# Optimization experiments

Hardware: AMD Instinct MI355X
Metric: run time of the kernel (lower is better)

## Reference

```python
import jax, jax.numpy as jnp
import numpy as np

N = 50000      # nodes
E = 800000     # edges
G = 32         # graphs in batch
K = 16         # max current nodes per graph
F_IN = 128
HID = 64
HEADS = 4
NEG = -1e9
TEMPERATURE = 1.0


def setup_inputs() -> dict:
    key = jax.random.key(0)
    ks = jax.random.split(key, 16)
    inp = {
        "x": jax.random.normal(ks[0], (N, F_IN), dtype=jnp.float32),
        "edge_index": jax.random.randint(ks[1], (2, E), 0, N, dtype=jnp.int64) if jax.config.jax_enable_x64 else jax.random.randint(ks[1], (2, E), 0, N).astype(jnp.int32),
        "cur_nodes": jax.random.randint(ks[2], (G, K), 0, N).astype(jnp.int32),
        "cur_counts": jax.random.randint(ks[3], (G,), 0, K).astype(jnp.int32),
        "masks": jax.random.bernoulli(ks[4], 0.3, (G, N)),
        "W1": jax.random.normal(ks[5], (F_IN, HEADS * HID), dtype=jnp.float32) * 0.05,
        "att_src1": jax.random.normal(ks[6], (HEADS, HID), dtype=jnp.float32) * 0.05,
        "att_dst1": jax.random.normal(ks[7], (HEADS, HID), dtype=jnp.float32) * 0.05,
        "b1": jax.random.normal(ks[8], (HEADS * HID,), dtype=jnp.float32) * 0.05,
        "W2": jax.random.normal(ks[9], (HEADS * HID, HID), dtype=jnp.float32) * 0.05,
        "att_src2": jax.random.normal(ks[10], (1, HID), dtype=jnp.float32) * 0.05,
        "att_dst2": jax.random.normal(ks[11], (1, HID), dtype=jnp.float32) * 0.05,
        "b2": jax.random.normal(ks[12], (HID,), dtype=jnp.float32) * 0.05,
        "action_w": jax.random.normal(ks[13], (HID, 1), dtype=jnp.float32) * 0.01,
        "action_b": jnp.zeros((1,), dtype=jnp.float32),
        "stop_w": jax.random.normal(ks[14], (HID, 1), dtype=jnp.float32) * 0.01,
        "stop_b": jnp.zeros((1,), dtype=jnp.float32),
    }
    return inp


def gat_conv(x, src, dst, W, att_s, att_d, b, num_nodes):
    """PyG-style GATConv (add_self_loops already applied to src/dst)."""
    H, C = att_s.shape
    h = (x @ W).reshape(num_nodes, H, C)            # [N,H,C]
    a_s = jnp.sum(h * att_s[None], axis=-1)         # [N,H]
    a_d = jnp.sum(h * att_d[None], axis=-1)         # [N,H]
    e = jax.nn.leaky_relu(a_s[src] + a_d[dst], 0.2) # [E',H]
    m = jax.ops.segment_max(e, dst, num_segments=num_nodes)
    ex = jnp.exp(e - m[dst])
    denom = jax.ops.segment_sum(ex, dst, num_segments=num_nodes)
    coef = ex / denom[dst]                          # scatter-softmax over dst
    out = jax.ops.segment_sum(coef[:, :, None] * h[src], dst, num_segments=num_nodes)
    return out.reshape(num_nodes, H * C) + b


def reference(x, edge_index, cur_nodes, cur_counts, masks,
              W1, att_src1, att_dst1, b1, W2, att_src2, att_dst2, b2,
              action_w, action_b, stop_w, stop_b):
    num_nodes = x.shape[0]
    loops = jnp.arange(num_nodes, dtype=edge_index.dtype)
    src = jnp.concatenate([edge_index[0], loops])
    dst = jnp.concatenate([edge_index[1], loops])

    h = jax.nn.relu(gat_conv(x, src, dst, W1, att_src1, att_dst1, b1, num_nodes))
    h = gat_conv(h, src, dst, W2, att_src2, att_dst2, b2, num_nodes)  # [N,HID]

    node_scores = jnp.tanh(h @ action_w + action_b)[:, 0]             # [N]

    # per-graph masked gather-mean pooling over current nodes
    valid = (jnp.arange(K)[None, :] < cur_counts[:, None])            # [G,K]
    gathered = h[cur_nodes] * valid[:, :, None].astype(h.dtype)       # [G,K,HID]
    cnt = jnp.maximum(cur_counts, 1).astype(h.dtype)
    contexts = gathered.sum(axis=1) / cnt[:, None]                    # [G,HID]
    stop_scores = jnp.tanh(contexts @ stop_w + stop_b)                # [G,1]

    masked = jnp.where(masks, node_scores[None, :], NEG)              # [G,N]
    all_scores = jnp.concatenate([masked, stop_scores], axis=1) / TEMPERATURE
    probs = jax.nn.softmax(all_scores, axis=-1)                       # [G,N+1]

    stop = (cur_counts == 0)
    onehot = jnp.zeros((num_nodes + 1,), dtype=probs.dtype).at[num_nodes].set(1.0)
    return jnp.where(stop[:, None], onehot[None, :], probs)
```

## Files before the change

kernel.cpp:

```cpp
#include <hip/hip_runtime.h>
#include <hip/hip_runtime_api.h>

#define NNODES 50000
#define NEDGES 800000
#define GG 32
#define KCUR 16
#define FIN 128
#define HIDN 64
#define NHEADS 4
#define F1 256
#define NCHUNK 196
#define NBUCK 196
#define EPB 2048

typedef unsigned short u16;
typedef unsigned char u8;
typedef short bf8 __attribute__((ext_vector_type(8)));
typedef float f32x4 __attribute__((ext_vector_type(4)));
typedef float f32x2 __attribute__((ext_vector_type(2)));

__device__ __forceinline__ u16 f2bf(float f) {
    unsigned u = __float_as_uint(f);
    return (u16)((u + 0x7fffu + ((u >> 16) & 1u)) >> 16);
}
__device__ __forceinline__ float lrelu(float x) { return x > 0.f ? x : 0.2f * x; }
__device__ __forceinline__ unsigned pk4fp8(float a, float b, float c, float d) {
    unsigned u = __builtin_amdgcn_cvt_pk_fp8_f32(a, b, 0u, false);
    u = __builtin_amdgcn_cvt_pk_fp8_f32(c, d, u, true);
    return u;
}

__device__ __forceinline__ void fma16(uint4 hv, float ex, float* acc) {
    f32x2 c;
    c = __builtin_amdgcn_cvt_pk_f32_fp8(hv.x, false);
    acc[0]  = fmaf(ex, c.x, acc[0]);  acc[1]  = fmaf(ex, c.y, acc[1]);
    c = __builtin_amdgcn_cvt_pk_f32_fp8(hv.x, true);
    acc[2]  = fmaf(ex, c.x, acc[2]);  acc[3]  = fmaf(ex, c.y, acc[3]);
    c = __builtin_amdgcn_cvt_pk_f32_fp8(hv.y, false);
    acc[4]  = fmaf(ex, c.x, acc[4]);  acc[5]  = fmaf(ex, c.y, acc[5]);
    c = __builtin_amdgcn_cvt_pk_f32_fp8(hv.y, true);
    acc[6]  = fmaf(ex, c.x, acc[6]);  acc[7]  = fmaf(ex, c.y, acc[7]);
    c = __builtin_amdgcn_cvt_pk_f32_fp8(hv.z, false);
    acc[8]  = fmaf(ex, c.x, acc[8]);  acc[9]  = fmaf(ex, c.y, acc[9]);
    c = __builtin_amdgcn_cvt_pk_f32_fp8(hv.z, true);
    acc[10] = fmaf(ex, c.x, acc[10]); acc[11] = fmaf(ex, c.y, acc[11]);
    c = __builtin_amdgcn_cvt_pk_f32_fp8(hv.w, false);
    acc[12] = fmaf(ex, c.x, acc[12]); acc[13] = fmaf(ex, c.y, acc[13]);
    c = __builtin_amdgcn_cvt_pk_f32_fp8(hv.w, true);
    acc[14] = fmaf(ex, c.x, acc[14]); acc[15] = fmaf(ex, c.y, acc[15]);
}

__device__ __forceinline__ void fma8(uint2 hv, float ex, float* acc) {
    f32x2 c;
    c = __builtin_amdgcn_cvt_pk_f32_fp8(hv.x, false);
    acc[0] = fmaf(ex, c.x, acc[0]); acc[1] = fmaf(ex, c.y, acc[1]);
    c = __builtin_amdgcn_cvt_pk_f32_fp8(hv.x, true);
    acc[2] = fmaf(ex, c.x, acc[2]); acc[3] = fmaf(ex, c.y, acc[3]);
    c = __builtin_amdgcn_cvt_pk_f32_fp8(hv.y, false);
    acc[4] = fmaf(ex, c.x, acc[4]); acc[5] = fmaf(ex, c.y, acc[5]);
    c = __builtin_amdgcn_cvt_pk_f32_fp8(hv.y, true);
    acc[6] = fmaf(ex, c.x, acc[6]); acc[7] = fmaf(ex, c.y, acc[7]);
}

__global__ __launch_bounds__(256)
void pack_k(const float* __restrict__ W1, const float* __restrict__ W2,
            u16* __restrict__ W1p, u16* __restrict__ W2p)
{
    int idx = blockIdx.x * 256 + threadIdx.x;
    const float* src; u16* dst; int S, N, li;
    if (idx < 32768) { src = W1; dst = W1p; S = FIN / 32; N = F1; li = idx; }
    else if (idx < 49152) { src = W2; dst = W2p; S = F1 / 32; N = HIDN; li = idx - 32768; }
    else return;
    int j = li & 7, l = (li >> 3) & 63, rest = li >> 9;
    int s = rest % S, t = rest / S;
    int k = s * 32 + (l >> 4) * 8 + j;
    int n = t * 16 + (l & 15);
    dst[li] = f2bf(src[(size_t)k * N + n]);
}

__global__ __launch_bounds__(256)
void hist_k(const int* __restrict__ dst, int* __restrict__ deg)
{
    int e = blockIdx.x * 256 + threadIdx.x;
    if (e >= NEDGES) return;
    atomicAdd(&deg[dst[e]], 1);
}

__global__ __launch_bounds__(256)
void chunksum_k(const int* __restrict__ deg, int* __restrict__ csum)
{
    __shared__ int ws[4];
    int i = blockIdx.x * 256 + threadIdx.x;
    int v = (i < NNODES) ? deg[i] : 0;
#pragma unroll
    for (int o = 32; o; o >>= 1) v += __shfl_down(v, o);
    if ((threadIdx.x & 63) == 0) ws[threadIdx.x >> 6] = v;
    __syncthreads();
    if (threadIdx.x == 0) csum[blockIdx.x] = ws[0] + ws[1] + ws[2] + ws[3];
}

__global__ __launch_bounds__(256)
void expand_k(const int* __restrict__ deg, const int* __restrict__ csum,
              int* __restrict__ rowptr, int* __restrict__ bcur)
{
    __shared__ int ws[4], ws2[4];
    __shared__ int boff;
    int tid = threadIdx.x, lane = tid & 63, wid = tid >> 6;
    int v0 = (tid < blockIdx.x) ? csum[tid] : 0;
#pragma unroll
    for (int o = 32; o; o >>= 1) v0 += __shfl_down(v0, o);
    if (lane == 0) ws[wid] = v0;
    __syncthreads();
    if (tid == 0) boff = ws[0] + ws[1] + ws[2] + ws[3];
    __syncthreads();
    int i = blockIdx.x * 256 + tid;
    int v = (i < NNODES) ? deg[i] : 0;
    int x = v;
#pragma unroll
    for (int o = 1; o < 64; o <<= 1) {
        int y = __shfl_up(x, o);
        if (lane >= o) x += y;
    }
    if (lane == 63) ws2[wid] = x;
    __syncthreads();
    int off = boff;
    for (int w = 0; w < wid; w++) off += ws2[w];
    int excl = off + x - v;
    if (i < NNODES) {
        rowptr[i] = excl;
        if ((i & 255) == 0) bcur[i >> 8] = excl;
    }
    if (i == 0) rowptr[NNODES] = NEDGES;
}

__global__ __launch_bounds__(256)
void bin_k(const int* __restrict__ src, const int* __restrict__ dst,
           int* __restrict__ bcur, uint2* __restrict__ tmp)
{
    __shared__ int lcnt[NBUCK];
    __shared__ int lbase[NBUCK];
    int tid = threadIdx.x;
    int e0 = blockIdx.x * EPB;
    for (int i = tid; i < NBUCK; i += 256) lcnt[i] = 0;
    __syncthreads();
    int s_[8], d_[8], r_[8];
#pragma unroll
    for (int j = 0; j < 8; j++) {
        int e = e0 + j * 256 + tid;
        if (e < NEDGES) {
            s_[j] = src[e];
            d_[j] = dst[e];
            r_[j] = atomicAdd(&lcnt[d_[j] >> 8], 1);
        }
    }
    __syncthreads();
    for (int i = tid; i < NBUCK; i += 256)
        if (lcnt[i]) lbase[i] = atomicAdd(&bcur[i], lcnt[i]);
    __syncthreads();
#pragma unroll
    for (int j = 0; j < 8; j++) {
        int e = e0 + j * 256 + tid;
        if (e < NEDGES) {
            int b = d_[j] >> 8;
            tmp[lbase[b] + r_[j]] = make_uint2((unsigned)s_[j], (unsigned)d_[j]);
        }
    }
}

__global__ __launch_bounds__(1024)
void reorder_k(const int* __restrict__ rowptr, const uint2* __restrict__ tmp,
               int* __restrict__ csr)
{
    __shared__ int cur[256];
    int tid = threadIdx.x;
    int b = blockIdx.x;
    int n0 = b << 8;
    if (tid < 256) {
        int n = n0 + tid;
        cur[tid] = (n < NNODES) ? rowptr[n] : 0;
    }
    int base = rowptr[n0];
    int end = (b == NBUCK - 1) ? NEDGES : rowptr[n0 + 256];
    __syncthreads();
    for (int e = base + tid; e < end; e += 1024) {
        uint2 pr = tmp[e];
        int pos = atomicAdd(&cur[pr.y & 255], 1);
        csr[pos] = (int)pr.x;
    }
}

__global__ __launch_bounds__(256)
void gemm1_k(const float* __restrict__ X, const u16* __restrict__ Bp,
             const float* __restrict__ att_s, const float* __restrict__ att_d,
             u8* __restrict__ h1f8, float* __restrict__ as1, float* __restrict__ ad1)
{
    const int S = FIN / 32;
    int lane = threadIdx.x & 63, w = threadIdx.x >> 6;
    int m0 = blockIdx.x * 64;
    int row_in = lane & 15, kq = lane >> 4;
    f32x4 acc[4][4];
#pragma unroll
    for (int r = 0; r < 4; r++)
#pragma unroll
        for (int tt = 0; tt < 4; tt++) acc[r][tt] = (f32x4){0.f, 0.f, 0.f, 0.f};
    int R = (NNODES - m0) >> 4; if (R > 4) R = 4;

    for (int s = 0; s < S; s++) {
        bf8 bfrag[4];
#pragma unroll
        for (int tt = 0; tt < 4; tt++) {
            int t = w * 4 + tt;
            bfrag[tt] = *(const bf8*)(Bp + (((size_t)t * S + s) * 64 + lane) * 8);
        }
        int kb = s * 32 + kq * 8;
        bf8 af[4];
#pragma unroll
        for (int r = 0; r < 4; r++)
            if (r < R) {
                const float* xp = X + (size_t)(m0 + r * 16 + row_in) * FIN + kb;
                float4 x0 = *(const float4*)xp;
                float4 x1 = *(const float4*)(xp + 4);
                bf8 a;
                a[0] = (short)f2bf(x0.x); a[1] = (short)f2bf(x0.y);
                a[2] = (short)f2bf(x0.z); a[3] = (short)f2bf(x0.w);
                a[4] = (short)f2bf(x1.x); a[5] = (short)f2bf(x1.y);
                a[6] = (short)f2bf(x1.z); a[7] = (short)f2bf(x1.w);
                af[r] = a;
            }
#pragma unroll
        for (int r = 0; r < 4; r++)
            if (r < R)
#pragma unroll
                for (int tt = 0; tt < 4; tt++)
                    acc[r][tt] = __builtin_amdgcn_mfma_f32_16x16x32_bf16(bfrag[tt], af[r], acc[r][tt], 0, 0, 0);
    }
    float attS[16], attD[16];
#pragma unroll
    for (int tt = 0; tt < 4; tt++)
#pragma unroll
        for (int v = 0; v < 4; v++) {
            attS[tt * 4 + v] = att_s[w * 64 + tt * 16 + kq * 4 + v];
            attD[tt * 4 + v] = att_d[w * 64 + tt * 16 + kq * 4 + v];
        }
#pragma unroll
    for (int r = 0; r < 4; r++) {
        if (r >= R) break;
        int node = m0 + r * 16 + row_in;
        float pa = 0.f, pd = 0.f;
#pragma unroll
        for (int tt = 0; tt < 4; tt++) {
            unsigned u = pk4fp8(acc[r][tt][0], acc[r][tt][1], acc[r][tt][2], acc[r][tt][3]);
            *(unsigned*)(h1f8 + (size_t)node * F1 + (w * 4 + tt) * 16 + kq * 4) = u;
#pragma unroll
            for (int v = 0; v < 4; v++) {
                pa = fmaf(acc[r][tt][v], attS[tt * 4 + v], pa);
                pd = fmaf(acc[r][tt][v], attD[tt * 4 + v], pd);
            }
        }
        pa += __shfl_xor(pa, 16); pa += __shfl_xor(pa, 32);
        pd += __shfl_xor(pd, 16); pd += __shfl_xor(pd, 32);
        if (kq == 0) { as1[node * 4 + w] = pa; ad1[node * 4 + w] = pd; }
    }
}

__global__ __launch_bounds__(256)
void gagg1_gemm2(const int* __restrict__ rowptr, const int* __restrict__ csr,
                 const float* __restrict__ as1, const float* __restrict__ ad1,
                 const u8* __restrict__ h1f8, const float* __restrict__ b1,
                 const u16* __restrict__ W2p,
                 const float* __restrict__ att_s, const float* __restrict__ att_d,
                 u8* __restrict__ h2f8, float* __restrict__ as2, float* __restrict__ ad2)
{
    __shared__ unsigned rows[16 * 128];
    __shared__ float asl[4][16], adl[4][16];
    int tid = threadIdx.x;
    int wid = tid >> 6, lane = tid & 63;
    int q = lane >> 4, li = lane & 15;
    int dl = wid * 4 + q;
    int d0 = blockIdx.x * 16;
    int d = d0 + dl;
    int beg = rowptr[d];
    int tot = rowptr[d + 1] - beg + 1;
    int h = li >> 2;
    int c0 = li << 4;
    const int* rowm = csr + beg - 1;
    float adh = ad1[d * 4 + h];
    float den = 0.f;
    float acc[16];
#pragma unroll
    for (int j = 0; j < 16; j++) acc[j] = 0.f;

    int s0 = d;
    int s1 = (1 < tot) ? rowm[1] : d;
    int s2 = (2 < tot) ? rowm[2] : d;
    int s3 = (3 < tot) ? rowm[3] : d;
    int p = 0;
    while (p < tot) {
        float av0 = as1[((unsigned)s0 << 2) + h];
        float av1 = as1[((unsigned)s1 << 2) + h];
        float av2 = as1[((unsigned)s2 << 2) + h];
        float av3 = as1[((unsigned)s3 << 2) + h];
        uint4 h0 = *(const uint4*)(h1f8 + ((unsigned)s0 << 8) + c0);
        uint4 h1 = *(const uint4*)(h1f8 + ((unsigned)s1 << 8) + c0);
        uint4 h2 = *(const uint4*)(h1f8 + ((unsigned)s2 << 8) + c0);
        uint4 h3 = *(const uint4*)(h1f8 + ((unsigned)s3 << 8) + c0);
        int np = p + 4;
        int n0 = (np     < tot) ? rowm[np]     : d;
        int n1 = (np + 1 < tot) ? rowm[np + 1] : d;
        int n2 = (np + 2 < tot) ? rowm[np + 2] : d;
        int n3 = (np + 3 < tot) ? rowm[np + 3] : d;
        float e0 = __expf(lrelu(av0 + adh));
        float e1 = (p + 1 < tot) ? __expf(lrelu(av1 + adh)) : 0.f;
        float e2 = (p + 2 < tot) ? __expf(lrelu(av2 + adh)) : 0.f;
        float e3 = (p + 3 < tot) ? __expf(lrelu(av3 + adh)) : 0.f;
        den += e0 + e1 + e2 + e3;
        fma16(h0, e0, acc);
        fma16(h1, e1, acc);
        fma16(h2, e2, acc);
        fma16(h3, e3, acc);
        s0 = n0; s1 = n1; s2 = n2; s3 = n3;
        p = np;
    }

    {
        float rden = 1.f / den;
        float4 b0 = *(const float4*)(b1 + c0);
        float4 b4 = *(const float4*)(b1 + c0 + 4);
        float4 b8 = *(const float4*)(b1 + c0 + 8);
        float4 bc = *(const float4*)(b1 + c0 + 12);
        float bb[16] = {b0.x, b0.y, b0.z, b0.w, b4.x, b4.y, b4.z, b4.w,
                        b8.x, b8.y, b8.z, b8.w, bc.x, bc.y, bc.z, bc.w};
        unsigned r[8];
#pragma unroll
        for (int jj = 0; jj < 8; jj++) {
            float lo = fmaxf(fmaf(acc[2 * jj],     rden, bb[2 * jj]),     0.f);
            float hi = fmaxf(fmaf(acc[2 * jj + 1], rden, bb[2 * jj + 1]), 0.f);
            asm("v_cvt_pk_bf16_f32 %0, %1, %2" : "=v"(r[jj]) : "v"(lo), "v"(hi));
        }
        unsigned* rb = rows + dl * 128;
        int g0 = (2 * li) ^ (dl & 7);
        int g1 = (2 * li + 1) ^ (dl & 7);
        *(uint4*)(rb + g0 * 4) = make_uint4(r[0], r[1], r[2], r[3]);
        *(uint4*)(rb + g1 * 4) = make_uint4(r[4], r[5], r[6], r[7]);
    }
    __syncthreads();

    int row_in = li, kq = q;
    f32x4 acc2 = (f32x4){0.f, 0.f, 0.f, 0.f};
#pragma unroll
    for (int s = 0; s < 8; s++) {
        bf8 bfrag = *(const bf8*)(W2p + (((size_t)wid * 8 + s) * 64 + lane) * 8);
        int g = (4 * s + kq) ^ (row_in & 7);
        bf8 af = *(const bf8*)(rows + row_in * 128 + g * 4);
        acc2 = __builtin_amdgcn_mfma_f32_16x16x32_bf16(bfrag, af, acc2, 0, 0, 0);
    }
    int node = d0 + row_in;
    unsigned u = pk4fp8(acc2[0], acc2[1], acc2[2], acc2[3]);
    *(unsigned*)(h2f8 + (size_t)node * HIDN + wid * 16 + kq * 4) = u;
    float pa = 0.f, pd = 0.f;
#pragma unroll
    for (int v = 0; v < 4; v++) {
        pa = fmaf(acc2[v], att_s[wid * 16 + kq * 4 + v], pa);
        pd = fmaf(acc2[v], att_d[wid * 16 + kq * 4 + v], pd);
    }
    pa += __shfl_xor(pa, 16); pa += __shfl_xor(pa, 32);
    pd += __shfl_xor(pd, 16); pd += __shfl_xor(pd, 32);
    if (kq == 0) { asl[wid][row_in] = pa; adl[wid][row_in] = pd; }
    __syncthreads();
    if (tid < 16) {
        as2[d0 + tid] = asl[0][tid] + asl[1][tid] + asl[2][tid] + asl[3][tid];
        ad2[d0 + tid] = adl[0][tid] + adl[1][tid] + adl[2][tid] + adl[3][tid];
    }
}

__global__ __launch_bounds__(256)
void gagg2(const int* __restrict__ rowptr, const int* __restrict__ csr,
           const float* __restrict__ as2, const float* __restrict__ ad2,
           const u8* __restrict__ h2f8, const float* __restrict__ b2,
           const float* __restrict__ aw, const float* __restrict__ ab,
           float* __restrict__ outp, float* __restrict__ scores)
{
    int wid = threadIdx.x >> 6, lane = threadIdx.x & 63;
    int d = blockIdx.x * 4 + wid;
    if (d >= NNODES) return;
    int beg = rowptr[d];
    int tot = rowptr[d + 1] - beg + 1;
    int g8 = lane >> 3;
    int li = lane & 7;
    int c0 = li << 3;
    const int* rowm = csr + beg - 1;
    float adh = ad2[d];
    float den = 0.f;
    float acc[8];
#pragma unroll
    for (int j = 0; j < 8; j++) acc[j] = 0.f;

    int p = g8;
    while (p + 8 < tot) {
        int sa = (p == 0) ? d : rowm[p];
        int sb = rowm[p + 8];
        float ava = as2[sa], avb = as2[sb];
        uint2 ha = *(const uint2*)(h2f8 + ((unsigned)sa << 6) + c0);
        uint2 hb = *(const uint2*)(h2f8 + ((unsigned)sb << 6) + c0);
        float exa = __expf(lrelu(ava + adh));
        den += exa;
        fma8(ha, exa, acc);
        float exb = __expf(lrelu(avb + adh));
        den += exb;
        fma8(hb, exb, acc);
        p += 16;
    }
    if (p < tot) {
        int s = (p == 0) ? d : rowm[p];
        float av = as2[s];
        uint2 hv = *(const uint2*)(h2f8 + ((unsigned)s << 6) + c0);
        float ex = __expf(lrelu(av + adh));
        den += ex;
        fma8(hv, ex, acc);
    }

    den += __shfl_xor(den, 8); den += __shfl_xor(den, 16); den += __shfl_xor(den, 32);
#pragma unroll
    for (int j = 0; j < 8; j++) {
        acc[j] += __shfl_xor(acc[j], 8);
        acc[j] += __shfl_xor(acc[j], 16);
        acc[j] += __shfl_xor(acc[j], 32);
    }

    float rden = 1.f / den;
    float4 blo = *(const float4*)(b2 + c0);
    float4 bhi = *(const float4*)(b2 + c0 + 4);
    float o0 = fmaf(acc[0], rden, blo.x);
    float o1 = fmaf(acc[1], rden, blo.y);
    float o2 = fmaf(acc[2], rden, blo.z);
    float o3 = fmaf(acc[3], rden, blo.w);
    float o4 = fmaf(acc[4], rden, bhi.x);
    float o5 = fmaf(acc[5], rden, bhi.y);
    float o6 = fmaf(acc[6], rden, bhi.z);
    float o7 = fmaf(acc[7], rden, bhi.w);
    if (lane < 8) {
        *(float4*)(outp + (size_t)d * HIDN + c0) = make_float4(o0, o1, o2, o3);
        *(float4*)(outp + (size_t)d * HIDN + c0 + 4) = make_float4(o4, o5, o6, o7);
    }
    float4 alo = *(const float4*)(aw + c0);
    float4 ahi = *(const float4*)(aw + c0 + 4);
    float p_ = o0 * alo.x + o1 * alo.y + o2 * alo.z + o3 * alo.w
             + o4 * ahi.x + o5 * ahi.y + o6 * ahi.z + o7 * ahi.w;
    p_ += __shfl_xor(p_, 1); p_ += __shfl_xor(p_, 2); p_ += __shfl_xor(p_, 4);
    if (lane == 0) scores[d] = tanhf(p_ + ab[0]);
}

__global__ __launch_bounds__(256)
void partials_k(const float* __restrict__ scores, const int* __restrict__ masks,
                float* __restrict__ pmax, float* __restrict__ psum)
{
    __shared__ float lm[4], ls[4];
    int g = blockIdx.y;
    float m = -3.0e38f, s = 0.f;
    for (int n = blockIdx.x * 256 + threadIdx.x; n < NNODES; n += gridDim.x * 256) {
        if (masks[(size_t)g * NNODES + n]) {
            float v = scores[n];
            if (v > m) { s = s * __expf(m - v) + 1.f; m = v; }
            else s += __expf(v - m);
        }
    }
#pragma unroll
    for (int o = 1; o < 64; o <<= 1) {
        float om = __shfl_xor(m, o), os = __shfl_xor(s, o);
        float M = fmaxf(m, om);
        s = s * __expf(m - M) + os * __expf(om - M);
        m = M;
    }
    if ((threadIdx.x & 63) == 0) { lm[threadIdx.x >> 6] = m; ls[threadIdx.x >> 6] = s; }
    __syncthreads();
    if (threadIdx.x == 0) {
        float M = m, S = s;
        for (int w_ = 1; w_ < 4; w_++) {
            float M2 = fmaxf(M, lm[w_]);
            S = S * __expf(M - M2) + ls[w_] * __expf(lm[w_] - M2);
            M = M2;
        }
        pmax[g * 64 + blockIdx.x] = M;
        psum[g * 64 + blockIdx.x] = S;
    }
}

__global__ __launch_bounds__(64)
void combine_k(const float* __restrict__ hf, const int* __restrict__ cur_nodes,
               const int* __restrict__ cur_counts, const float* __restrict__ sw,
               const float* __restrict__ sb,
               const float* __restrict__ pmax, const float* __restrict__ psum,
               float* __restrict__ gmax, float* __restrict__ gsum,
               float* __restrict__ stops)
{
    int g = blockIdx.x, tid = threadIdx.x;
    int cnt = cur_counts[g];
    float s = 0.f;
    for (int k = 0; k < KCUR; k++)
        if (k < cnt) s += hf[(size_t)cur_nodes[g * KCUR + k] * HIDN + tid];
    float ctx = s / (float)(cnt > 1 ? cnt : 1);
    float p = ctx * sw[tid];
#pragma unroll
    for (int o = 1; o < 64; o <<= 1) p += __shfl_xor(p, o);
    float stop = tanhf(p + sb[0]);

    float m = pmax[g * 64 + tid], sm = psum[g * 64 + tid];
#pragma unroll
    for (int o = 1; o < 64; o <<= 1) {
        float om = __shfl_xor(m, o), os = __shfl_xor(sm, o);
        float M = fmaxf(m, om);
        sm = sm * __expf(m - M) + os * __expf(om - M);
        m = M;
    }
    if (tid == 0) {
        float M2 = fmaxf(m, stop);
        float S2 = sm * __expf(m - M2) + __expf(stop - M2);
        gmax[g] = M2; gsum[g] = S2; stops[g] = stop;
    }
}

__global__ __launch_bounds__(256)
void write_k(const float* __restrict__ scores, const int* __restrict__ masks,
             const float* __restrict__ gmax, const float* __restrict__ gsum,
             const float* __restrict__ stops, const int* __restrict__ cur_counts,
             float* __restrict__ out)
{
    int g = blockIdx.y;
    int j = blockIdx.x * 256 + threadIdx.x;
    if (j > NNODES) return;
    float v;
    if (cur_counts[g] == 0) {
        v = (j == NNODES) ? 1.f : 0.f;
    } else {
        float m = gmax[g];
        float Z = gsum[g];
        if (j == NNODES) v = __expf(stops[g] - m) / Z;
        else v = masks[(size_t)g * NNODES + j] ? __expf(scores[j] - m) / Z : 0.f;
    }
    out[(size_t)g * (NNODES + 1) + j] = v;
}

extern "C" void kernel_launch(void* const* d_in, const int* in_sizes, int n_in,
                              void* d_out, int out_size, void* d_ws, size_t ws_size,
                              hipStream_t stream) {
    const float* x        = (const float*)d_in[0];
    const int* ei         = (const int*)d_in[1];
    const int* cur_nodes  = (const int*)d_in[2];
    const int* cur_counts = (const int*)d_in[3];
    const int* masks      = (const int*)d_in[4];
    const float* W1       = (const float*)d_in[5];
    const float* att_s1   = (const float*)d_in[6];
    const float* att_d1   = (const float*)d_in[7];
    const float* b1       = (const float*)d_in[8];
    const float* W2       = (const float*)d_in[9];
    const float* att_s2   = (const float*)d_in[10];
    const float* att_d2   = (const float*)d_in[11];
    const float* b2       = (const float*)d_in[12];
    const float* action_w = (const float*)d_in[13];
    const float* action_b = (const float*)d_in[14];
    const float* stop_w   = (const float*)d_in[15];
    const float* stop_b   = (const float*)d_in[16];
    float* out = (float*)d_out;

    const int* srcp = ei;
    const int* dstp = ei + NEDGES;

    int* deg = (int*)d_ws;
    char* zend = (char*)(deg + NNODES);
    size_t zbytes = zend - (char*)d_ws;
    int* csum   = (int*)zend;
    int* rowptr = csum + 256;
    int* bcur   = rowptr + NNODES + 4;
    int* csr    = bcur + 256;
    u16* W1p    = (u16*)(csr + NEDGES);
    u16* W2p    = W1p + 32768;
    u8*  h1f8   = (u8*)(W2p + 16384);
    u8*  h2f8   = h1f8 + (size_t)NNODES * F1;
    float* as1  = (float*)(h2f8 + (size_t)NNODES * HIDN);
    float* ad1  = as1 + (size_t)NNODES * 4;
    float* as2  = ad1 + (size_t)NNODES * 4;
    float* ad2  = as2 + NNODES;
    float* hf   = ad2 + NNODES;
    float* scores = hf + (size_t)NNODES * HIDN;
    float* stops  = scores + NNODES;
    float* pmax = stops + GG;
    float* psum = pmax + GG * 64;
    float* gmax = psum + GG * 64;
    float* gsum = gmax + GG;
    size_t total = (char*)(gsum + GG) - (char*)d_ws;
    if (total > ws_size) return;

    uint2* tmp = (uint2*)hf;

    auto cdiv = [](long long a, long long b) { return (int)((a + b - 1) / b); };

    (void)hipMemsetAsync(deg, 0, zbytes, stream);

    hist_k<<<cdiv(NEDGES, 256), 256, 0, stream>>>(dstp, deg);
    chunksum_k<<<NCHUNK, 256, 0, stream>>>(deg, csum);
    expand_k<<<NCHUNK, 256, 0, stream>>>(deg, csum, rowptr, bcur);
    bin_k<<<cdiv(NEDGES, EPB), 256, 0, stream>>>(srcp, dstp, bcur, tmp);
    reorder_k<<<NBUCK, 1024, 0, stream>>>(rowptr, tmp, csr);

    pack_k<<<192, 256, 0, stream>>>(W1, W2, W1p, W2p);

    gemm1_k<<<cdiv(NNODES, 64), 256, 0, stream>>>(x, W1p, att_s1, att_d1, h1f8, as1, ad1);

    gagg1_gemm2<<<NNODES / 16, 256, 0, stream>>>(rowptr, csr, as1, ad1, h1f8, b1,
                                                 W2p, att_s2, att_d2, h2f8, as2, ad2);

    gagg2<<<cdiv(NNODES, 4), 256, 0, stream>>>(rowptr, csr, as2, ad2, h2f8, b2,
                                               action_w, action_b, hf, scores);

    partials_k<<<dim3(64, GG), 256, 0, stream>>>(scores, masks, pmax, psum);
    combine_k<<<GG, 64, 0, stream>>>(hf, cur_nodes, cur_counts, stop_w, stop_b,
                                     pmax, psum, gmax, gsum, stops);
    write_k<<<dim3(cdiv(NNODES + 1, 256), GG), 256, 0, stream>>>(scores, masks, gmax, gsum,
                                                                 stops, cur_counts, out);
}
```

Measured before the change: 282.4 us.

## Sort destination nodes by degree to balance aggregation work per block

Builds a degree histogram and counting-sort order of nodes, then has both aggregation kernels process nodes in that order, so that the nodes grouped into each block and wavefront have similar edge counts. This is meant to reduce load imbalance and divergence in the per-node edge loops. It adds two small kernels, an extra indirection on node index, and scattered writes of outputs instead of contiguous ones. The atomic-based ordering within a bin is nondeterministic but still covers every node exactly once.

```diff
diff --git a/kernel.cpp b/kernel.cpp
--- a/kernel.cpp
+++ b/kernel.cpp
@@ -12,6 +12,7 @@
 #define NCHUNK 196
 #define NBUCK 196
 #define EPB 2048
+#define DBIN 64
 
 typedef unsigned short u16;
 typedef unsigned char u8;
@@ -87,16 +88,52 @@
 }
 
 __global__ __launch_bounds__(256)
-void chunksum_k(const int* __restrict__ deg, int* __restrict__ csum)
+void chunksum_k(const int* __restrict__ deg, int* __restrict__ csum,
+                int* __restrict__ dhist)
 {
     __shared__ int ws[4];
+    __shared__ int lh[DBIN];
+    int tid = threadIdx.x;
+    if (tid < DBIN) lh[tid] = 0;
+    __syncthreads();
+    int i = blockIdx.x * 256 + tid;
+    int v = 0;
+    if (i < NNODES) {
+        v = deg[i];
+        atomicAdd(&lh[v < DBIN - 1 ? v : DBIN - 1], 1);
+    }
+#pragma unroll
+    for (int o = 32; o; o >>= 1) v += __shfl_down(v, o);
+    if ((tid & 63) == 0) ws[tid >> 6] = v;
+    __syncthreads();
+    if (tid == 0) csum[blockIdx.x] = ws[0] + ws[1] + ws[2] + ws[3];
+    if (tid < DBIN && lh[tid]) atomicAdd(&dhist[tid], lh[tid]);
+}
+
+__global__ __launch_bounds__(64)
+void dprefix_k(const int* __restrict__ dhist, int* __restrict__ dcur)
+{
+    int tid = threadIdx.x;
+    int v = dhist[tid];
+    int x = v;
+#pragma unroll
+    for (int o = 1; o < 64; o <<= 1) {
+        int y = __shfl_up(x, o);
+        if (tid >= o) x += y;
+    }
+    dcur[tid] = x - v;
+}
+
+__global__ __launch_bounds__(256)
+void dorder_k(const int* __restrict__ deg, int* __restrict__ dcur,
+              int* __restrict__ order)
+{
     int i = blockIdx.x * 256 + threadIdx.x;
-    int v = (i < NNODES) ? deg[i] : 0;
-#pragma unroll
-    for (int o = 32; o; o >>= 1) v += __shfl_down(v, o);
-    if ((threadIdx.x & 63) == 0) ws[threadIdx.x >> 6] = v;
-    __syncthreads();
-    if (threadIdx.x == 0) csum[blockIdx.x] = ws[0] + ws[1] + ws[2] + ws[3];
+    if (i >= NNODES) return;
+    int v = deg[i];
+    int b = v < DBIN - 1 ? v : DBIN - 1;
+    int pos = atomicAdd(&dcur[b], 1);
+    order[pos] = i;
 }
 
 __global__ __launch_bounds__(256)
@@ -264,7 +301,8 @@
 }
 
 __global__ __launch_bounds__(256)
-void gagg1_gemm2(const int* __restrict__ rowptr, const int* __restrict__ csr,
+void gagg1_gemm2(const int* __restrict__ order,
+                 const int* __restrict__ rowptr, const int* __restrict__ csr,
                  const float* __restrict__ as1, const float* __restrict__ ad1,
                  const u8* __restrict__ h1f8, const float* __restrict__ b1,
                  const u16* __restrict__ W2p,
@@ -278,7 +316,7 @@
     int q = lane >> 4, li = lane & 15;
     int dl = wid * 4 + q;
     int d0 = blockIdx.x * 16;
-    int d = d0 + dl;
+    int d = order[d0 + dl];
     int beg = rowptr[d];
     int tot = rowptr[d + 1] - beg + 1;
     int h = li >> 2;
@@ -346,6 +384,7 @@
     __syncthreads();
 
     int row_in = li, kq = q;
+    int nodeB = order[d0 + row_in];
     f32x4 acc2 = (f32x4){0.f, 0.f, 0.f, 0.f};
 #pragma unroll
     for (int s = 0; s < 8; s++) {
@@ -354,9 +393,8 @@
         bf8 af = *(const bf8*)(rows + row_in * 128 + g * 4);
         acc2 = __builtin_amdgcn_mfma_f32_16x16x32_bf16(bfrag, af, acc2, 0, 0, 0);
     }
-    int node = d0 + row_in;
     unsigned u = pk4fp8(acc2[0], acc2[1], acc2[2], acc2[3]);
-    *(unsigned*)(h2f8 + (size_t)node * HIDN + wid * 16 + kq * 4) = u;
+    *(unsigned*)(h2f8 + (size_t)nodeB * HIDN + wid * 16 + kq * 4) = u;
     float pa = 0.f, pd = 0.f;
 #pragma unroll
     for (int v = 0; v < 4; v++) {
@@ -368,21 +406,22 @@
     if (kq == 0) { asl[wid][row_in] = pa; adl[wid][row_in] = pd; }
     __syncthreads();
     if (tid < 16) {
-        as2[d0 + tid] = asl[0][tid] + asl[1][tid] + asl[2][tid] + asl[3][tid];
-        ad2[d0 + tid] = adl[0][tid] + adl[1][tid] + adl[2][tid] + adl[3][tid];
-    }
-}
-
-__global__ __launch_bounds__(256)
-void gagg2(const int* __restrict__ rowptr, const int* __restrict__ csr,
+        int nd = order[d0 + tid];
+        as2[nd] = asl[0][tid] + asl[1][tid] + asl[2][tid] + asl[3][tid];
+        ad2[nd] = adl[0][tid] + adl[1][tid] + adl[2][tid] + adl[3][tid];
+    }
+}
+
+__global__ __launch_bounds__(256)
+void gagg2(const int* __restrict__ order,
+           const int* __restrict__ rowptr, const int* __restrict__ csr,
            const float* __restrict__ as2, const float* __restrict__ ad2,
            const u8* __restrict__ h2f8, const float* __restrict__ b2,
            const float* __restrict__ aw, const float* __restrict__ ab,
            float* __restrict__ outp, float* __restrict__ scores)
 {
     int wid = threadIdx.x >> 6, lane = threadIdx.x & 63;
-    int d = blockIdx.x * 4 + wid;
-    if (d >= NNODES) return;
+    int d = order[blockIdx.x * 4 + wid];
     int beg = rowptr[d];
     int tot = rowptr[d + 1] - beg + 1;
     int g8 = lane >> 3;
@@ -566,12 +605,15 @@
     const int* dstp = ei + NEDGES;
 
     int* deg = (int*)d_ws;
-    char* zend = (char*)(deg + NNODES);
+    int* dhist = deg + NNODES;
+    char* zend = (char*)(dhist + DBIN);
     size_t zbytes = zend - (char*)d_ws;
     int* csum   = (int*)zend;
     int* rowptr = csum + 256;
     int* bcur   = rowptr + NNODES + 4;
-    int* csr    = bcur + 256;
+    int* dcur   = bcur + 256;
+    int* order  = dcur + DBIN;
+    int* csr    = order + NNODES;
     u16* W1p    = (u16*)(csr + NEDGES);
     u16* W2p    = W1p + 32768;
     u8*  h1f8   = (u8*)(W2p + 16384);
@@ -597,19 +639,21 @@
     (void)hipMemsetAsync(deg, 0, zbytes, stream);
 
     hist_k<<<cdiv(NEDGES, 256), 256, 0, stream>>>(dstp, deg);
-    chunksum_k<<<NCHUNK, 256, 0, stream>>>(deg, csum);
+    chunksum_k<<<NCHUNK, 256, 0, stream>>>(deg, csum, dhist);
     expand_k<<<NCHUNK, 256, 0, stream>>>(deg, csum, rowptr, bcur);
     bin_k<<<cdiv(NEDGES, EPB), 256, 0, stream>>>(srcp, dstp, bcur, tmp);
     reorder_k<<<NBUCK, 1024, 0, stream>>>(rowptr, tmp, csr);
+    dprefix_k<<<1, 64, 0, stream>>>(dhist, dcur);
+    dorder_k<<<NCHUNK, 256, 0, stream>>>(deg, dcur, order);
 
     pack_k<<<192, 256, 0, stream>>>(W1, W2, W1p, W2p);
 
     gemm1_k<<<cdiv(NNODES, 64), 256, 0, stream>>>(x, W1p, att_s1, att_d1, h1f8, as1, ad1);
 
-    gagg1_gemm2<<<NNODES / 16, 256, 0, stream>>>(rowptr, csr, as1, ad1, h1f8, b1,
+    gagg1_gemm2<<<NNODES / 16, 256, 0, stream>>>(order, rowptr, csr, as1, ad1, h1f8, b1,
                                                  W2p, att_s2, att_d2, h2f8, as2, ad2);
 
-    gagg2<<<cdiv(NNODES, 4), 256, 0, stream>>>(rowptr, csr, as2, ad2, h2f8, b2,
+    gagg2<<<cdiv(NNODES, 4), 256, 0, stream>>>(order, rowptr, csr, as2, ad2, h2f8, b2,
                                                action_w, action_b, hf, scores);
 
     partials_k<<<dim3(64, GG), 256, 0, stream>>>(scores, masks, pmax, psum);
```

Result: slower. 443.9 us (+57.2%).

## Merge CSR build, weight pack, GEMM1 and softmax head into cooperative persistent kernels

Applied to the files above, without the earlier changes.

Replaces the memset, histogram, scan, bin, reorder, pack and gemm1 launches with one cooperative kernel that uses grid-wide syncs between phases. The GEMM1 tiles overlap with the degree histogram inside the same phase. The three softmax-head kernels are likewise fused into one cooperative kernel with grid syncs. Buckets shrink to 128 nodes so there are enough blocks to fill the 512-block grid. This removes per-launch overhead and idle gaps between kernels, at the cost of grid.sync latency and a fixed grid of 512 blocks that relies on 2 blocks fitting per CU.

```diff
diff --git a/kernel.cpp b/kernel.cpp
--- a/kernel.cpp
+++ b/kernel.cpp
@@ -1,5 +1,8 @@
 #include <hip/hip_runtime.h>
 #include <hip/hip_runtime_api.h>
+#include <hip/hip_cooperative_groups.h>
+
+namespace cg = cooperative_groups;
 
 #define NNODES 50000
 #define NEDGES 800000
@@ -10,8 +13,10 @@
 #define NHEADS 4
 #define F1 256
 #define NCHUNK 196
-#define NBUCK 196
-#define EPB 2048
+#define NBUCKR 391
+#define CBLK 512
+#define CTHR (CBLK*256)
+#define EPB2 1563
 
 typedef unsigned short u16;
 typedef unsigned char u8;
@@ -62,141 +67,14 @@
     acc[6] = fmaf(ex, c.x, acc[6]); acc[7] = fmaf(ex, c.y, acc[7]);
 }
 
-__global__ __launch_bounds__(256)
-void pack_k(const float* __restrict__ W1, const float* __restrict__ W2,
-            u16* __restrict__ W1p, u16* __restrict__ W2p)
-{
-    int idx = blockIdx.x * 256 + threadIdx.x;
-    const float* src; u16* dst; int S, N, li;
-    if (idx < 32768) { src = W1; dst = W1p; S = FIN / 32; N = F1; li = idx; }
-    else if (idx < 49152) { src = W2; dst = W2p; S = F1 / 32; N = HIDN; li = idx - 32768; }
-    else return;
-    int j = li & 7, l = (li >> 3) & 63, rest = li >> 9;
-    int s = rest % S, t = rest / S;
-    int k = s * 32 + (l >> 4) * 8 + j;
-    int n = t * 16 + (l & 15);
-    dst[li] = f2bf(src[(size_t)k * N + n]);
-}
-
-__global__ __launch_bounds__(256)
-void hist_k(const int* __restrict__ dst, int* __restrict__ deg)
-{
-    int e = blockIdx.x * 256 + threadIdx.x;
-    if (e >= NEDGES) return;
-    atomicAdd(&deg[dst[e]], 1);
-}
-
-__global__ __launch_bounds__(256)
-void chunksum_k(const int* __restrict__ deg, int* __restrict__ csum)
-{
-    __shared__ int ws[4];
-    int i = blockIdx.x * 256 + threadIdx.x;
-    int v = (i < NNODES) ? deg[i] : 0;
-#pragma unroll
-    for (int o = 32; o; o >>= 1) v += __shfl_down(v, o);
-    if ((threadIdx.x & 63) == 0) ws[threadIdx.x >> 6] = v;
-    __syncthreads();
-    if (threadIdx.x == 0) csum[blockIdx.x] = ws[0] + ws[1] + ws[2] + ws[3];
-}
-
-__global__ __launch_bounds__(256)
-void expand_k(const int* __restrict__ deg, const int* __restrict__ csum,
-              int* __restrict__ rowptr, int* __restrict__ bcur)
-{
-    __shared__ int ws[4], ws2[4];
-    __shared__ int boff;
-    int tid = threadIdx.x, lane = tid & 63, wid = tid >> 6;
-    int v0 = (tid < blockIdx.x) ? csum[tid] : 0;
-#pragma unroll
-    for (int o = 32; o; o >>= 1) v0 += __shfl_down(v0, o);
-    if (lane == 0) ws[wid] = v0;
-    __syncthreads();
-    if (tid == 0) boff = ws[0] + ws[1] + ws[2] + ws[3];
-    __syncthreads();
-    int i = blockIdx.x * 256 + tid;
-    int v = (i < NNODES) ? deg[i] : 0;
-    int x = v;
-#pragma unroll
-    for (int o = 1; o < 64; o <<= 1) {
-        int y = __shfl_up(x, o);
-        if (lane >= o) x += y;
-    }
-    if (lane == 63) ws2[wid] = x;
-    __syncthreads();
-    int off = boff;
-    for (int w = 0; w < wid; w++) off += ws2[w];
-    int excl = off + x - v;
-    if (i < NNODES) {
-        rowptr[i] = excl;
-        if ((i & 255) == 0) bcur[i >> 8] = excl;
-    }
-    if (i == 0) rowptr[NNODES] = NEDGES;
-}
-
-__global__ __launch_bounds__(256)
-void bin_k(const int* __restrict__ src, const int* __restrict__ dst,
-           int* __restrict__ bcur, uint2* __restrict__ tmp)
-{
-    __shared__ int lcnt[NBUCK];
-    __shared__ int lbase[NBUCK];
-    int tid = threadIdx.x;
-    int e0 = blockIdx.x * EPB;
-    for (int i = tid; i < NBUCK; i += 256) lcnt[i] = 0;
-    __syncthreads();
-    int s_[8], d_[8], r_[8];
-#pragma unroll
-    for (int j = 0; j < 8; j++) {
-        int e = e0 + j * 256 + tid;
-        if (e < NEDGES) {
-            s_[j] = src[e];
-            d_[j] = dst[e];
-            r_[j] = atomicAdd(&lcnt[d_[j] >> 8], 1);
-        }
-    }
-    __syncthreads();
-    for (int i = tid; i < NBUCK; i += 256)
-        if (lcnt[i]) lbase[i] = atomicAdd(&bcur[i], lcnt[i]);
-    __syncthreads();
-#pragma unroll
-    for (int j = 0; j < 8; j++) {
-        int e = e0 + j * 256 + tid;
-        if (e < NEDGES) {
-            int b = d_[j] >> 8;
-            tmp[lbase[b] + r_[j]] = make_uint2((unsigned)s_[j], (unsigned)d_[j]);
-        }
-    }
-}
-
-__global__ __launch_bounds__(1024)
-void reorder_k(const int* __restrict__ rowptr, const uint2* __restrict__ tmp,
-               int* __restrict__ csr)
-{
-    __shared__ int cur[256];
-    int tid = threadIdx.x;
-    int b = blockIdx.x;
-    int n0 = b << 8;
-    if (tid < 256) {
-        int n = n0 + tid;
-        cur[tid] = (n < NNODES) ? rowptr[n] : 0;
-    }
-    int base = rowptr[n0];
-    int end = (b == NBUCK - 1) ? NEDGES : rowptr[n0 + 256];
-    __syncthreads();
-    for (int e = base + tid; e < end; e += 1024) {
-        uint2 pr = tmp[e];
-        int pos = atomicAdd(&cur[pr.y & 255], 1);
-        csr[pos] = (int)pr.x;
-    }
-}
-
-__global__ __launch_bounds__(256)
-void gemm1_k(const float* __restrict__ X, const u16* __restrict__ Bp,
-             const float* __restrict__ att_s, const float* __restrict__ att_d,
-             u8* __restrict__ h1f8, float* __restrict__ as1, float* __restrict__ ad1)
+__device__ void gemm1_tile(int m0, const float* __restrict__ X,
+                           const u16* __restrict__ Bp,
+                           const float* __restrict__ att_s, const float* __restrict__ att_d,
+                           u8* __restrict__ h1f8, float* __restrict__ as1,
+                           float* __restrict__ ad1, int tid)
 {
     const int S = FIN / 32;
-    int lane = threadIdx.x & 63, w = threadIdx.x >> 6;
-    int m0 = blockIdx.x * 64;
+    int lane = tid & 63, w = tid >> 6;
     int row_in = lane & 15, kq = lane >> 4;
     f32x4 acc[4][4];
 #pragma unroll
@@ -260,6 +138,131 @@
         pa += __shfl_xor(pa, 16); pa += __shfl_xor(pa, 32);
         pd += __shfl_xor(pd, 16); pd += __shfl_xor(pd, 32);
         if (kq == 0) { as1[node * 4 + w] = pa; ad1[node * 4 + w] = pd; }
+    }
+}
+
+__global__ __launch_bounds__(256, 2)
+void build_k(const float* __restrict__ W1, const float* __restrict__ W2,
+             u16* __restrict__ W1p, u16* __restrict__ W2p,
+             const float* __restrict__ X,
+             const float* __restrict__ att_s1, const float* __restrict__ att_d1,
+             u8* __restrict__ h1f8, float* __restrict__ as1, float* __restrict__ ad1,
+             const int* __restrict__ srcp, const int* __restrict__ dstp,
+             int* __restrict__ deg, int* __restrict__ csum,
+             int* __restrict__ rowptr, int* __restrict__ bcur,
+             uint2* __restrict__ tmp, int* __restrict__ csr)
+{
+    cg::grid_group grid = cg::this_grid();
+    __shared__ int lcnt[NBUCKR];
+    __shared__ int lbase[NBUCKR];
+    __shared__ int ws[4], ws2[4];
+    __shared__ int boff;
+    __shared__ int cur[128];
+    int bid = blockIdx.x, tid = threadIdx.x;
+    int gtid = bid * 256 + tid;
+
+    if (gtid < 49152) {
+        const float* src; u16* dst; int S, N, li;
+        if (gtid < 32768) { src = W1; dst = W1p; S = FIN / 32; N = F1; li = gtid; }
+        else { src = W2; dst = W2p; S = F1 / 32; N = HIDN; li = gtid - 32768; }
+        int j = li & 7, l = (li >> 3) & 63, rest = li >> 9;
+        int s = rest % S, t = rest / S;
+        int k = s * 32 + (l >> 4) * 8 + j;
+        int n = t * 16 + (l & 15);
+        dst[li] = f2bf(src[(size_t)k * N + n]);
+    }
+    if (gtid < NNODES) deg[gtid] = 0;
+    grid.sync();
+
+    for (int t = bid; t < (NNODES + 63) / 64; t += CBLK)
+        gemm1_tile(t * 64, X, W1p, att_s1, att_d1, h1f8, as1, ad1, tid);
+    for (int e = gtid; e < NEDGES; e += CTHR)
+        atomicAdd(&deg[dstp[e]], 1);
+    grid.sync();
+
+    if (bid < NCHUNK) {
+        int i = bid * 256 + tid;
+        int v = (i < NNODES) ? deg[i] : 0;
+#pragma unroll
+        for (int o = 32; o; o >>= 1) v += __shfl_down(v, o);
+        if ((tid & 63) == 0) ws[tid >> 6] = v;
+        __syncthreads();
+        if (tid == 0) csum[bid] = ws[0] + ws[1] + ws[2] + ws[3];
+    }
+    grid.sync();
+
+    if (bid < NCHUNK) {
+        int lane = tid & 63, wid = tid >> 6;
+        int v0 = (tid < bid) ? csum[tid] : 0;
+#pragma unroll
+        for (int o = 32; o; o >>= 1) v0 += __shfl_down(v0, o);
+        if (lane == 0) ws[wid] = v0;
+        __syncthreads();
+        if (tid == 0) boff = ws[0] + ws[1] + ws[2] + ws[3];
+        __syncthreads();
+        int i = bid * 256 + tid;
+        int v = (i < NNODES) ? deg[i] : 0;
+        int x = v;
+#pragma unroll
+        for (int o = 1; o < 64; o <<= 1) {
+            int y = __shfl_up(x, o);
+            if (lane >= o) x += y;
+        }
+        if (lane == 63) ws2[wid] = x;
+        __syncthreads();
+        int off = boff;
+        for (int w = 0; w < wid; w++) off += ws2[w];
+        int excl = off + x - v;
+        if (i < NNODES) {
+            rowptr[i] = excl;
+            if ((i & 127) == 0) bcur[i >> 7] = excl;
+        }
+        if (i == 0) rowptr[NNODES] = NEDGES;
+    }
+    grid.sync();
+
+    {
+        int e0 = bid * EPB2;
+        for (int i = tid; i < NBUCKR; i += 256) lcnt[i] = 0;
+        __syncthreads();
+        int s_[7], d_[7], r_[7];
+#pragma unroll
+        for (int j = 0; j < 7; j++) {
+            int e = e0 + j * 256 + tid;
+            if (j * 256 + tid < EPB2 && e < NEDGES) {
+                s_[j] = srcp[e];
+                d_[j] = dstp[e];
+                r_[j] = atomicAdd(&lcnt[d_[j] >> 7], 1);
+            } else d_[j] = -1;
+        }
+        __syncthreads();
+        for (int i = tid; i < NBUCKR; i += 256)
+            if (lcnt[i]) lbase[i] = atomicAdd(&bcur[i], lcnt[i]);
+        __syncthreads();
+#pragma unroll
+        for (int j = 0; j < 7; j++) {
+            if (d_[j] >= 0) {
+                int b = d_[j] >> 7;
+                tmp[lbase[b] + r_[j]] = make_uint2((unsigned)s_[j], (unsigned)d_[j]);
+            }
+        }
+    }
+    grid.sync();
+
+    if (bid < NBUCKR) {
+        int n0 = bid << 7;
+        if (tid < 128) {
+            int n = n0 + tid;
+            cur[tid] = (n < NNODES) ? rowptr[n] : 0;
+        }
+        int base = rowptr[n0];
+        int end = (bid == NBUCKR - 1) ? NEDGES : rowptr[n0 + 128];
+        __syncthreads();
+        for (int e = base + tid; e < end; e += 256) {
+            uint2 pr = tmp[e];
+            int pos = atomicAdd(&cur[pr.y & 127], 1);
+            csr[pos] = (int)pr.x;
+        }
     }
 }
 
@@ -450,94 +453,99 @@
     if (lane == 0) scores[d] = tanhf(p_ + ab[0]);
 }
 
-__global__ __launch_bounds__(256)
-void partials_k(const float* __restrict__ scores, const int* __restrict__ masks,
-                float* __restrict__ pmax, float* __restrict__ psum)
+__global__ __launch_bounds__(256, 2)
+void head_k(const float* __restrict__ scores, const int* __restrict__ masks,
+            const float* __restrict__ hf, const int* __restrict__ cur_nodes,
+            const int* __restrict__ cur_counts,
+            const float* __restrict__ sw, const float* __restrict__ sb,
+            float* __restrict__ pmax, float* __restrict__ psum,
+            float* __restrict__ gmax, float* __restrict__ gsum,
+            float* __restrict__ stops, float* __restrict__ out)
 {
+    cg::grid_group grid = cg::this_grid();
     __shared__ float lm[4], ls[4];
-    int g = blockIdx.y;
-    float m = -3.0e38f, s = 0.f;
-    for (int n = blockIdx.x * 256 + threadIdx.x; n < NNODES; n += gridDim.x * 256) {
-        if (masks[(size_t)g * NNODES + n]) {
-            float v = scores[n];
-            if (v > m) { s = s * __expf(m - v) + 1.f; m = v; }
-            else s += __expf(v - m);
-        }
-    }
-#pragma unroll
-    for (int o = 1; o < 64; o <<= 1) {
-        float om = __shfl_xor(m, o), os = __shfl_xor(s, o);
-        float M = fmaxf(m, om);
-        s = s * __expf(m - M) + os * __expf(om - M);
-        m = M;
-    }
-    if ((threadIdx.x & 63) == 0) { lm[threadIdx.x >> 6] = m; ls[threadIdx.x >> 6] = s; }
-    __syncthreads();
-    if (threadIdx.x == 0) {
-        float M = m, S = s;
-        for (int w_ = 1; w_ < 4; w_++) {
-            float M2 = fmaxf(M, lm[w_]);
-            S = S * __expf(M - M2) + ls[w_] * __expf(lm[w_] - M2);
-            M = M2;
-        }
-        pmax[g * 64 + blockIdx.x] = M;
-        psum[g * 64 + blockIdx.x] = S;
-    }
-}
-
-__global__ __launch_bounds__(64)
-void combine_k(const float* __restrict__ hf, const int* __restrict__ cur_nodes,
-               const int* __restrict__ cur_counts, const float* __restrict__ sw,
-               const float* __restrict__ sb,
-               const float* __restrict__ pmax, const float* __restrict__ psum,
-               float* __restrict__ gmax, float* __restrict__ gsum,
-               float* __restrict__ stops)
-{
-    int g = blockIdx.x, tid = threadIdx.x;
-    int cnt = cur_counts[g];
-    float s = 0.f;
-    for (int k = 0; k < KCUR; k++)
-        if (k < cnt) s += hf[(size_t)cur_nodes[g * KCUR + k] * HIDN + tid];
-    float ctx = s / (float)(cnt > 1 ? cnt : 1);
-    float p = ctx * sw[tid];
-#pragma unroll
-    for (int o = 1; o < 64; o <<= 1) p += __shfl_xor(p, o);
-    float stop = tanhf(p + sb[0]);
-
-    float m = pmax[g * 64 + tid], sm = psum[g * 64 + tid];
-#pragma unroll
-    for (int o = 1; o < 64; o <<= 1) {
-        float om = __shfl_xor(m, o), os = __shfl_xor(sm, o);
-        float M = fmaxf(m, om);
-        sm = sm * __expf(m - M) + os * __expf(om - M);
-        m = M;
-    }
-    if (tid == 0) {
-        float M2 = fmaxf(m, stop);
-        float S2 = sm * __expf(m - M2) + __expf(stop - M2);
-        gmax[g] = M2; gsum[g] = S2; stops[g] = stop;
-    }
-}
-
-__global__ __launch_bounds__(256)
-void write_k(const float* __restrict__ scores, const int* __restrict__ masks,
-             const float* __restrict__ gmax, const float* __restrict__ gsum,
-             const float* __restrict__ stops, const int* __restrict__ cur_counts,
-             float* __restrict__ out)
-{
-    int g = blockIdx.y;
-    int j = blockIdx.x * 256 + threadIdx.x;
-    if (j > NNODES) return;
-    float v;
-    if (cur_counts[g] == 0) {
-        v = (j == NNODES) ? 1.f : 0.f;
-    } else {
-        float m = gmax[g];
-        float Z = gsum[g];
-        if (j == NNODES) v = __expf(stops[g] - m) / Z;
-        else v = masks[(size_t)g * NNODES + j] ? __expf(scores[j] - m) / Z : 0.f;
-    }
-    out[(size_t)g * (NNODES + 1) + j] = v;
+    int bid = blockIdx.x, tid = threadIdx.x;
+    int gtid = bid * 256 + tid;
+
+    {
+        int g = bid >> 4, c = bid & 15;
+        int n0 = c * 3125;
+        float m = -3.0e38f, s = 0.f;
+        for (int n = n0 + tid; n < n0 + 3125; n += 256) {
+            if (masks[(size_t)g * NNODES + n]) {
+                float v = scores[n];
+                if (v > m) { s = s * __expf(m - v) + 1.f; m = v; }
+                else s += __expf(v - m);
+            }
+        }
+#pragma unroll
+        for (int o = 1; o < 64; o <<= 1) {
+            float om = __shfl_xor(m, o), os = __shfl_xor(s, o);
+            float M = fmaxf(m, om);
+            s = s * __expf(m - M) + os * __expf(om - M);
+            m = M;
+        }
+        if ((tid & 63) == 0) { lm[tid >> 6] = m; ls[tid >> 6] = s; }
+        __syncthreads();
+        if (tid == 0) {
+            float M = m, S = s;
+            for (int w_ = 1; w_ < 4; w_++) {
+                float M2 = fmaxf(M, lm[w_]);
+                S = S * __expf(M - M2) + ls[w_] * __expf(lm[w_] - M2);
+                M = M2;
+            }
+            pmax[g * 16 + c] = M;
+            psum[g * 16 + c] = S;
+        }
+    }
+    grid.sync();
+
+    if (bid < GG && tid < 64) {
+        int g = bid;
+        int cnt = cur_counts[g];
+        float s = 0.f;
+        for (int k = 0; k < KCUR; k++)
+            if (k < cnt) s += hf[(size_t)cur_nodes[g * KCUR + k] * HIDN + tid];
+        float ctx = s / (float)(cnt > 1 ? cnt : 1);
+        float p = ctx * sw[tid];
+#pragma unroll
+        for (int o = 1; o < 64; o <<= 1) p += __shfl_xor(p, o);
+        float stop = tanhf(p + sb[0]);
+
+        float m = (tid < 16) ? pmax[g * 16 + tid] : -3.0e38f;
+        float sm = (tid < 16) ? psum[g * 16 + tid] : 0.f;
+#pragma unroll
+        for (int o = 1; o < 64; o <<= 1) {
+            float om = __shfl_xor(m, o), os = __shfl_xor(sm, o);
+            float M = fmaxf(m, om);
+            sm = sm * __expf(m - M) + os * __expf(om - M);
+            m = M;
+        }
+        if (tid == 0) {
+            float M2 = fmaxf(m, stop);
+            float S2 = sm * __expf(m - M2) + __expf(stop - M2);
+            gmax[g] = M2; gsum[g] = S2; stops[g] = stop;
+        }
+    }
+    grid.sync();
+
+    {
+        const int total = GG * (NNODES + 1);
+        for (int w = gtid; w < total; w += CTHR) {
+            int g = w / (NNODES + 1);
+            int j = w - g * (NNODES + 1);
+            float v;
+            if (cur_counts[g] == 0) {
+                v = (j == NNODES) ? 1.f : 0.f;
+            } else {
+                float m = gmax[g];
+                float Z = gsum[g];
+                if (j == NNODES) v = __expf(stops[g] - m) / Z;
+                else v = masks[(size_t)g * NNODES + j] ? __expf(scores[j] - m) / Z : 0.f;
+            }
+            out[w] = v;
+        }
+    }
 }
 
 extern "C" void kernel_launch(void* const* d_in, const int* in_sizes, int n_in,
@@ -566,12 +574,10 @@
     const int* dstp = ei + NEDGES;
 
     int* deg = (int*)d_ws;
-    char* zend = (char*)(deg + NNODES);
-    size_t zbytes = zend - (char*)d_ws;
-    int* csum   = (int*)zend;
+    int* csum   = deg + NNODES;
     int* rowptr = csum + 256;
     int* bcur   = rowptr + NNODES + 4;
-    int* csr    = bcur + 256;
+    int* csr    = bcur + 400;
     u16* W1p    = (u16*)(csr + NEDGES);
     u16* W2p    = W1p + 32768;
     u8*  h1f8   = (u8*)(W2p + 16384);
@@ -584,8 +590,8 @@
     float* scores = hf + (size_t)NNODES * HIDN;
     float* stops  = scores + NNODES;
     float* pmax = stops + GG;
-    float* psum = pmax + GG * 64;
-    float* gmax = psum + GG * 64;
+    float* psum = pmax + GG * 16;
+    float* gmax = psum + GG * 16;
     float* gsum = gmax + GG;
     size_t total = (char*)(gsum + GG) - (char*)d_ws;
     if (total > ws_size) return;
@@ -594,17 +600,18 @@
 
     auto cdiv = [](long long a, long long b) { return (int)((a + b - 1) / b); };
 
-    (void)hipMemsetAsync(deg, 0, zbytes, stream);
-
-    hist_k<<<cdiv(NEDGES, 256), 256, 0, stream>>>(dstp, deg);
-    chunksum_k<<<NCHUNK, 256, 0, stream>>>(deg, csum);
-    expand_k<<<NCHUNK, 256, 0, stream>>>(deg, csum, rowptr, bcur);
-    bin_k<<<cdiv(NEDGES, EPB), 256, 0, stream>>>(srcp, dstp, bcur, tmp);
-    reorder_k<<<NBUCK, 1024, 0, stream>>>(rowptr, tmp, csr);
-
-    pack_k<<<192, 256, 0, stream>>>(W1, W2, W1p, W2p);
-
-    gemm1_k<<<cdiv(NNODES, 64), 256, 0, stream>>>(x, W1p, att_s1, att_d1, h1f8, as1, ad1);
+    {
+        void* args[] = {
+            (void*)&W1, (void*)&W2, (void*)&W1p, (void*)&W2p,
+            (void*)&x, (void*)&att_s1, (void*)&att_d1,
+            (void*)&h1f8, (void*)&as1, (void*)&ad1,
+            (void*)&srcp, (void*)&dstp,
+            (void*)&deg, (void*)&csum, (void*)&rowptr, (void*)&bcur,
+            (void*)&tmp, (void*)&csr
+        };
+        (void)hipLaunchCooperativeKernel((void*)build_k, dim3(CBLK), dim3(256),
+                                         args, 0, stream);
+    }
 
     gagg1_gemm2<<<NNODES / 16, 256, 0, stream>>>(rowptr, csr, as1, ad1, h1f8, b1,
                                                  W2p, att_s2, att_d2, h2f8, as2, ad2);
@@ -612,9 +619,15 @@
     gagg2<<<cdiv(NNODES, 4), 256, 0, stream>>>(rowptr, csr, as2, ad2, h2f8, b2,
                                                action_w, action_b, hf, scores);
 
-    partials_k<<<dim3(64, GG), 256, 0, stream>>>(scores, masks, pmax, psum);
-    combine_k<<<GG, 64, 0, stream>>>(hf, cur_nodes, cur_counts, stop_w, stop_b,
-                                     pmax, psum, gmax, gsum, stops);
-    write_k<<<dim3(cdiv(NNODES + 1, 256), GG), 256, 0, stream>>>(scores, masks, gmax, gsum,
-                                                                 stops, cur_counts, out);
-}
+    {
+        void* args[] = {
+            (void*)&scores, (void*)&masks, (void*)&hf,
+            (void*)&cur_nodes, (void*)&cur_counts,
+            (void*)&stop_w, (void*)&stop_b,
+            (void*)&pmax, (void*)&psum, (void*)&gmax, (void*)&gsum,
+            (void*)&stops, (void*)&out
+        };
+        (void)hipLaunchCooperativeKernel((void*)head_k, dim3(CBLK), dim3(256),
+                                         args, 0, stream);
+    }
+}
```

New measurement: 660.1 us. 134% more time.
